# Kernel optimization log

Measured on AMD Instinct MI355X. Metric: run time of the kernel, lower is better.

The kernel has to match this reference:

```python
import jax, jax.numpy as jnp
import numpy as np
from jax import lax

B, L = 16384, 32
HID, CIN = 8, 2
N_SUB = 2            # RK4 substeps per spline interval (fixed-step stand-in for torchcde's adaptive solver)
T10_LO, T10_HI = 0.1, 7.0


def push_zeros(a):
    # torch: move nonzero entries of each row to the right end, zeros to the left.
    # stable ascending sort on validity key (0 for zeros, 1 for valid) reproduces this exactly
    # because the invalid entries are exactly 0.
    keys = (a != 0).astype(jnp.int32)
    order = jnp.argsort(keys, axis=1)  # jax sorts are stable
    return jnp.take_along_axis(a, order, axis=1)


def setup_inputs() -> dict:
    key = jax.random.key(0)
    ks = jax.random.split(key, 12)
    fa_len = jax.random.randint(ks[0], (B, 1), L // 2, L + 1)          # 16..32 valid points
    valid = jnp.arange(L)[None, :] < fa_len                             # (B, L)
    X_fa_in = jnp.where(valid, jax.random.uniform(ks[1], (B, L), minval=0.1, maxval=1.1), 0.0)
    fa_vals_in = jnp.where(valid, jax.random.uniform(ks[2], (B, L), minval=0.05, maxval=0.45), 0.0)
    TR_vals = jax.random.uniform(ks[3], (B, 1), minval=0.003, maxval=0.01)
    fa_mask = valid

    def lin(k, fout, fin):
        kw, kb = jax.random.split(k)
        s = 1.0 / np.sqrt(fin)
        return (jax.random.uniform(kw, (fout, fin), minval=-s, maxval=s),
                jax.random.uniform(kb, (fout,), minval=-s, maxval=s))

    W_init, b_init = lin(ks[4], HID, CIN)        # self.initial: Linear(2, 8)
    W1, b1 = lin(ks[5], 256, HID)                # CDE_Func.linear1
    W2, b2 = lin(ks[6], CIN * HID, 256)          # CDE_Func.linear2
    Wr1, br1 = lin(ks[7], 200, HID)              # reg_T10
    Wr2, br2 = lin(ks[8], 200, 200)
    Wr3, br3 = lin(ks[9], 1, 200)
    return dict(X_fa_in=X_fa_in, fa_vals_in=fa_vals_in, TR_vals=TR_vals,
                W_init=W_init, b_init=b_init, W1=W1, b1=b1, W2=W2, b2=b2,
                Wr1=Wr1, br1=br1, Wr2=Wr2, br2=br2, Wr3=Wr3, br3=br3,
                fa_mask=fa_mask, fa_len=fa_len)


def _forward(X_fa_in, fa_vals_in, TR_vals, W_init, b_init, W1, b1, W2, b2,
             Wr1, br1, Wr2, br2, Wr3, br3, fa_mask, fa_len):
    fl = fa_len[:, 0]                       # (B,) int
    fl_f = fl.astype(X_fa_in.dtype)
    mean = jnp.sum(X_fa_in, axis=1) / fl_f
    Xn = X_fa_in / mean[:, None]
    X_fa = push_zeros(Xn)
    fa_vals = push_zeros(fa_vals_in)
    bidx = jnp.arange(X_fa.shape[0])
    last_X = X_fa[bidx, fl - 1][:, None]            # pushed array indexed at fa_len-1 (as in torch)
    last_fa = fa_vals_in[bidx, fl - 1][:, None]     # original array indexed at fa_len-1
    X_fa = jnp.where(X_fa == 0.0, last_X, X_fa)
    fa_vals = jnp.where(fa_vals == 0.0, last_fa, fa_vals)
    x = jnp.stack([fa_vals, X_fa], axis=-1)         # (B, L, 2): channels (fa, X)

    # Hermite cubic with backward differences, unit knot spacing t_i = i
    diffs = x[:, 1:] - x[:, :-1]                    # (B, L-1, C)
    m = jnp.concatenate([diffs[:, :1], diffs], axis=1)  # m_0 = fwd diff, m_i = backward diff
    X0s, X1s = x[:, :-1], x[:, 1:]                  # per-interval knot values (B, L-1, C)
    M0s, M1s = m[:, :-1], m[:, 1:]

    z0 = x[:, 0] @ W_init.T + b_init                # X.evaluate(interval[0]) == first knot

    def f(z):  # CDE vector field: (B, HID) -> (B, HID, CIN)
        h = jax.nn.relu(z @ W1.T + b1)
        g = jnp.tanh(h @ W2.T + b2)
        return g.reshape(z.shape[0], HID, CIN)

    hstep = 1.0 / N_SUB
    nI = x.shape[1] - 1
    intervals = jnp.repeat(jnp.arange(nI), N_SUB)
    s0s = jnp.tile(jnp.arange(N_SUB) * hstep, nI).astype(x.dtype)

    def step(z, ts):
        i, s0 = ts
        x0, x1 = X0s[:, i], X1s[:, i]
        m0, m1 = M0s[:, i], M1s[:, i]

        def dX(s):  # spline derivative dX/dt at local coord s in [0,1]
            s2 = s * s
            return ((6 * s2 - 6 * s) * x0 + (3 * s2 - 4 * s + 1) * m0 +
                    (-6 * s2 + 6 * s) * x1 + (3 * s2 - 2 * s) * m1)

        def F(s, zz):
            return jnp.einsum('bhc,bc->bh', f(zz), dX(s))

        k1 = F(s0, z)
        k2 = F(s0 + hstep / 2, z + 0.5 * hstep * k1)
        k3 = F(s0 + hstep / 2, z + 0.5 * hstep * k2)
        k4 = F(s0 + hstep, z + hstep * k3)
        return z + (hstep / 6) * (k1 + 2 * k2 + 2 * k3 + k4), None

    z_T, _ = lax.scan(step, z0, (intervals, s0s))

    h1 = jax.nn.gelu(z_T @ Wr1.T + br1, approximate=False)
    h2 = jax.nn.gelu(h1 @ Wr2.T + br2, approximate=False)
    t = (h2 @ Wr3.T + br3)[:, 0]
    T10 = T10_LO + jax.nn.sigmoid(t)[:, None] * (T10_HI - T10_LO)   # (B, 1)
    R1 = 1.0 / T10
    E = jnp.exp(-TR_vals * R1)                                      # (B, 1)
    X_out = (1 - E) * jnp.sin(fa_vals_in) / (1 - jnp.cos(fa_vals_in) * E)
    mean2 = jnp.sum(X_out, axis=1) / fl_f
    X_out = X_out / mean2[:, None]
    M0 = jnp.ones_like(T10)
    return X_out, T10, M0


def reference(X_fa_in, fa_vals_in, TR_vals, W_init, b_init, W1, b1, W2, b2,
              Wr1, br1, Wr2, br2, Wr3, br3, fa_mask, fa_len):
    return _forward(X_fa_in, fa_vals_in, TR_vals, W_init, b_init, W1, b1, W2, b2,
                    Wr1, br1, Wr2, br2, Wr3, br3, fa_mask, fa_len)
```

## Files before the change

kernel.cpp:

```cpp
#include <hip/hip_runtime.h>
#include <hip/hip_bf16.h>

#define B_ROWS 16384
#define L_SEQ  32

typedef _Float16 f16;
typedef __attribute__((ext_vector_type(4))) _Float16 f16x4;
typedef __attribute__((ext_vector_type(8))) _Float16 f16x8;
typedef __attribute__((ext_vector_type(4))) float f32x4;
typedef __attribute__((ext_vector_type(4))) unsigned int u32x4;

__device__ __forceinline__ unsigned pkh(float a, float b) {
    return __builtin_bit_cast(unsigned, __builtin_amdgcn_cvt_pkrtz(a, b));
}
__device__ __forceinline__ float tanh_fast(float x) {
    float e = __expf(2.0f * x);
    float r = __builtin_amdgcn_rcpf(e + 1.0f);
    return fmaf(-2.0f, r, 1.0f);
}
__device__ __forceinline__ float gelu_exact(float x) {
    return 0.5f * x * (1.0f + erff(x * 0.70710678118654752440f));
}
__device__ __forceinline__ void pin2(uint2& v) {
    unsigned x0 = v.x, x1 = v.y;
    asm volatile("" : "+v"(x0), "+v"(x1));
    v = make_uint2(x0, x1);
}
__device__ __forceinline__ void pin4(u32x4& v) {
    unsigned x0 = v[0], x1 = v[1], x2 = v[2], x3 = v[3];
    asm volatile("" : "+v"(x0), "+v"(x1), "+v"(x2), "+v"(x3));
    v = (u32x4){x0, x1, x2, x3};
}

__global__ __launch_bounds__(256, 2) void fused_kernel(
    const float* __restrict__ Xin, const float* __restrict__ Fin,
    const float* __restrict__ TRv,
    const int*   __restrict__ fa_len,
    const float* __restrict__ Wi,  const float* __restrict__ bi,
    const float* __restrict__ W1g, const float* __restrict__ b1g,
    const float* __restrict__ W2g, const float* __restrict__ b2g,
    const float* __restrict__ Wr1, const float* __restrict__ br1,
    const float* __restrict__ Wr2, const float* __restrict__ br2,
    const float* __restrict__ Wr3, const float* __restrict__ br3,
    float* __restrict__ out)
{
    __shared__ __align__(16) float xm[32 * 132];
    __shared__ __align__(16) f32x4 exch[2][2][2][64];
    __shared__ float texch[2][2][16];
#define XM(r_, i_, c_) xm[(r_) * 132 + (i_) * 4 + (c_)]

    const int tid = threadIdx.x;
    const int g16 = tid >> 4, sub = tid & 15;

    float mean_r[2]; int fl_r[2];
#pragma unroll
    for (int r = 0; r < 2; ++r) {
        const int row_l = g16 * 2 + r;
        const int row   = blockIdx.x * 32 + row_l;
        const float* Xr = Xin + row * L_SEQ;
        const float* Fr = Fin + row * L_SEQ;
        float xr0 = Xr[sub], xr1 = Xr[sub + 16];
        float fr0 = Fr[sub], fr1 = Fr[sub + 16];
        fl_r[r] = fa_len[row];
        float s = xr0 + xr1;
        s += __shfl_xor(s, 1, 16);
        s += __shfl_xor(s, 2, 16);
        s += __shfl_xor(s, 4, 16);
        s += __shfl_xor(s, 8, 16);
        mean_r[r] = s / (float)fl_r[r];
        XM(row_l, sub, 0)      = fr0; XM(row_l, sub, 1)      = xr0;
        XM(row_l, sub + 16, 0) = fr1; XM(row_l, sub + 16, 1) = xr1;
    }
    __syncthreads();

    float ff[2][2], xf[2][2];
#pragma unroll
    for (int r = 0; r < 2; ++r) {
        const int row_l = g16 * 2 + r;
        const int fl = fl_r[r];
        const float mean = mean_r[r];
        const int shift = L_SEQ - fl;
        int lsrc  = fl - 1 - shift;
        int lsrcC = lsrc < 0 ? 0 : lsrc;
        float lastX = (lsrc >= 0) ? (XM(row_l, lsrcC, 1) / mean) : 0.0f;
        float lastF = XM(row_l, fl - 1, 0);
#pragma unroll
        for (int u = 0; u < 2; ++u) {
            int p = sub + u * 16;
            int src = p - shift;
            int sc  = src < 0 ? 0 : src;
            float fraw = XM(row_l, sc, 0);
            float xraw = XM(row_l, sc, 1);
            ff[r][u] = (src >= 0) ? fraw : lastF;
            xf[r][u] = (src >= 0) ? (xraw / mean) : lastX;
        }
    }
    __syncthreads();
#pragma unroll
    for (int r = 0; r < 2; ++r) {
        const int row_l = g16 * 2 + r;
#pragma unroll
        for (int u = 0; u < 2; ++u) {
            int p = sub + u * 16;
            XM(row_l, p, 0) = ff[r][u];
            XM(row_l, p, 1) = xf[r][u];
        }
    }
    __syncthreads();
#pragma unroll
    for (int r = 0; r < 2; ++r) {
        const int row_l = g16 * 2 + r;
#pragma unroll
        for (int u = 0; u < 2; ++u) {
            int p = sub + u * 16;
            int qd = (p == 0) ? 1 : p;
            XM(row_l, p, 2) = XM(row_l, qd, 0) - XM(row_l, qd - 1, 0);
            XM(row_l, p, 3) = XM(row_l, qd, 1) - XM(row_l, qd - 1, 1);
        }
    }
    __syncthreads();

    const int wv   = tid >> 6;
    const int lane = tid & 63;
    const int pairId = wv >> 1;
    const int half   = wv & 1;
    const int n    = lane & 15;
    const int q    = lane >> 4;
    const int rowl = pairId * 16 + n;
    const int rowg = blockIdx.x * 32 + rowl;

    uint2 a1[8];
#pragma unroll
    for (int tt = 0; tt < 8; ++tt) {
        const int t = 8 * half + tt;
        const float* wr = W1g + (t * 16 + n) * 8 + (q < 2 ? q * 4 : 0);
        float4 w4 = *(const float4*)wr;
        float b1v = b1g[t * 16 + n];
        unsigned d0 = (q < 2) ? pkh(w4.x, w4.y) : (q == 2 ? pkh(b1v, 0.0f) : 0u);
        unsigned d1 = (q < 2) ? pkh(w4.z, w4.w) : 0u;
        a1[tt] = make_uint2(d0, d1);
        pin2(a1[tt]);
    }
    u32x4 a2[4];
#pragma unroll
    for (int tt = 0; tt < 4; ++tt) {
        const int kk = 4 * half + tt;
        const float* w2r = W2g + n * 256 + kk * 32 + 4 * q;
        float4 p0 = *(const float4*)(w2r);
        float4 p1 = *(const float4*)(w2r + 16);
        a2[tt] = (u32x4){pkh(p0.x, p0.y), pkh(p0.z, p0.w), pkh(p1.x, p1.y), pkh(p1.z, p1.w)};
        pin4(a2[tt]);
    }
    f32x4 c2seed;
#pragma unroll
    for (int r = 0; r < 4; ++r) c2seed[r] = (half == 0) ? b2g[4 * q + r] : 0.0f;

    float f0 = XM(rowl, 0, 0), X0 = XM(rowl, 0, 1);
    float z0 = fmaf(Wi[(2 * q) * 2], f0, fmaf(Wi[(2 * q) * 2 + 1], X0, bi[2 * q]));
    float z1 = fmaf(Wi[(2 * q + 1) * 2], f0, fmaf(Wi[(2 * q + 1) * 2 + 1], X0, bi[2 * q + 1]));

    const int bpi = (((q & 1) << 5) + n) << 2;
    const f32x4 zero4 = {0.f, 0.f, 0.f, 0.f};
    const f16x8 zf16 = {0, 0, 0, 0, 0, 0, 0, 0};

    auto make_bz = [&](float zza, float zzb) -> uint2 {
        unsigned myz = pkh(zza, zzb);
        int b0 = __builtin_amdgcn_ds_bpermute(bpi, (int)myz);
        int b1 = __builtin_amdgcn_ds_bpermute(bpi + 64, (int)myz);
        unsigned bz0 = (q < 2) ? (unsigned)b0 : (q == 2 ? 0x3C00u : 0u);
        unsigned bz1 = (q < 2) ? (unsigned)b1 : 0u;
        return make_uint2(bz0, bz1);
    };

    auto FEVAL = [&](int ph, float zza, float zzb, float d0c, float d1c,
                     float& ko0, float& ko1) {
        uint2 bzp = make_bz(zza, zzb);
        f16x4 bz = __builtin_bit_cast(f16x4, bzp);

        f32x4 c1[8];
#pragma unroll
        for (int tt = 0; tt < 8; ++tt)
            c1[tt] = __builtin_amdgcn_mfma_f32_16x16x16f16(
                __builtin_bit_cast(f16x4, a1[tt]), bz, zero4, 0, 0, 0);

        f16x8 hf[4];
#pragma unroll
        for (int tt = 0; tt < 4; ++tt) {
            u32x4 w = (u32x4){pkh(c1[2 * tt][0],     c1[2 * tt][1]),
                              pkh(c1[2 * tt][2],     c1[2 * tt][3]),
                              pkh(c1[2 * tt + 1][0], c1[2 * tt + 1][1]),
                              pkh(c1[2 * tt + 1][2], c1[2 * tt + 1][3])};
            hf[tt] = __builtin_elementwise_max(__builtin_bit_cast(f16x8, w), zf16);
        }

        f32x4 c2a = c2seed, c2b = zero4;
        c2a = __builtin_amdgcn_mfma_f32_16x16x32_f16(
            __builtin_bit_cast(f16x8, a2[0]), hf[0], c2a, 0, 0, 0);
        c2b = __builtin_amdgcn_mfma_f32_16x16x32_f16(
            __builtin_bit_cast(f16x8, a2[2]), hf[2], c2b, 0, 0, 0);
        c2a = __builtin_amdgcn_mfma_f32_16x16x32_f16(
            __builtin_bit_cast(f16x8, a2[1]), hf[1], c2a, 0, 0, 0);
        c2b = __builtin_amdgcn_mfma_f32_16x16x32_f16(
            __builtin_bit_cast(f16x8, a2[3]), hf[3], c2b, 0, 0, 0);
        f32x4 Gp = c2a + c2b;

        exch[pairId][ph][half][lane] = Gp;
        __syncthreads();
        f32x4 G = Gp + exch[pairId][ph][half ^ 1][lane];

        float t0 = tanh_fast(G[0]), t1 = tanh_fast(G[1]);
        float t2 = tanh_fast(G[2]), t3 = tanh_fast(G[3]);
        ko0 = fmaf(t0, d0c, t1 * d1c);
        ko1 = fmaf(t2, d0c, t3 * d1c);
    };

    int ph = 0;
#pragma unroll 1
    for (int i = 0; i < 31; ++i) {
        float4 P0 = *(const float4*)&XM(rowl, i, 0);
        float4 P1 = *(const float4*)&XM(rowl, i + 1, 0);
        float m0f = P0.z, m0X = P0.w, m1f = P1.z, m1X = P1.w;
        float df  = P0.x - P1.x, dXx = P0.y - P1.y;

        float d25f = fmaf(-1.125f, df,  fmaf(0.1875f, m0f, -0.3125f * m1f));
        float d25X = fmaf(-1.125f, dXx, fmaf(0.1875f, m0X, -0.3125f * m1X));
        float d50f = fmaf(-1.5f,   df,  fmaf(-0.25f,  m0f, -0.25f   * m1f));
        float d50X = fmaf(-1.5f,   dXx, fmaf(-0.25f,  m0X, -0.25f   * m1X));
        float d75f = fmaf(-1.125f, df,  fmaf(-0.3125f, m0f, 0.1875f * m1f));
        float d75X = fmaf(-1.125f, dXx, fmaf(-0.3125f, m0X, 0.1875f * m1X));

#pragma unroll 1
        for (int ssi = 0; ssi < 2; ++ssi) {
            float daf = ssi ? d50f : m0f,  daX = ssi ? d50X : m0X;
            float dbf = ssi ? d75f : d25f, dbX = ssi ? d75X : d25X;
            float ddf = ssi ? m1f  : d50f, ddX = ssi ? m1X  : d50X;

            float k1a, k1b, k2a, k2b, k3a, k3b, k4a, k4b, zza, zzb;
            FEVAL(ph, z0, z1, daf, daX, k1a, k1b);       ph ^= 1;
            zza = fmaf(0.25f, k1a, z0); zzb = fmaf(0.25f, k1b, z1);
            FEVAL(ph, zza, zzb, dbf, dbX, k2a, k2b);     ph ^= 1;
            zza = fmaf(0.25f, k2a, z0); zzb = fmaf(0.25f, k2b, z1);
            FEVAL(ph, zza, zzb, dbf, dbX, k3a, k3b);     ph ^= 1;
            zza = fmaf(0.5f, k3a, z0);  zzb = fmaf(0.5f, k3b, z1);
            FEVAL(ph, zza, zzb, ddf, ddX, k4a, k4b);     ph ^= 1;

            float ka = fmaf(2.f, k2a, k1a); ka = fmaf(2.f, k3a, ka);
            float kb = fmaf(2.f, k2b, k1b); kb = fmaf(2.f, k3b, kb);
            z0 = fmaf(1.f / 12.f, ka + k4a, z0);
            z1 = fmaf(1.f / 12.f, kb + k4b, z1);
        }
    }

    uint2 bzp = make_bz(z0, z1);
    f16x4 bzr = __builtin_bit_cast(f16x4, bzp);
    f32x4 c1r[13];
#pragma unroll
    for (int t = 0; t < 13; ++t) {
        int m = 16 * t + n;
        uint2 afp = make_uint2(0u, 0u);
        if (q < 2) {
            if (m < 200) {
                float4 w4 = *(const float4*)(Wr1 + m * 8 + 4 * q);
                afp = make_uint2(pkh(w4.x, w4.y), pkh(w4.z, w4.w));
            }
        } else if (q == 2) {
            float b = (m < 200) ? br1[m] : 0.0f;
            afp.x = pkh(b, 0.0f);
        }
        c1r[t] = __builtin_amdgcn_mfma_f32_16x16x16f16(
            __builtin_bit_cast(f16x4, afp), bzr, zero4, 0, 0, 0);
    }

    f16x8 hf2[7];
#pragma unroll
    for (int kk = 0; kk < 7; ++kk) {
        float g0 = gelu_exact(c1r[2 * kk][0]), g1 = gelu_exact(c1r[2 * kk][1]);
        float g2 = gelu_exact(c1r[2 * kk][2]), g3 = gelu_exact(c1r[2 * kk][3]);
        float g4 = 0.f, g5 = 0.f, g6 = 0.f, g7 = 0.f;
        if (kk < 6) {
            g4 = gelu_exact(c1r[2 * kk + 1][0]); g5 = gelu_exact(c1r[2 * kk + 1][1]);
            g6 = gelu_exact(c1r[2 * kk + 1][2]); g7 = gelu_exact(c1r[2 * kk + 1][3]);
        }
        u32x4 w = (u32x4){pkh(g0, g1), pkh(g2, g3), pkh(g4, g5), pkh(g6, g7)};
        hf2[kk] = __builtin_bit_cast(f16x8, w);
    }

    float tpart = 0.0f;
    const int mt0 = half * 7, mt1 = half ? 13 : 7;
#pragma unroll 1
    for (int mt = mt0; mt < mt1; ++mt) {
        int mb = 16 * mt + 4 * q;
        f32x4 c2 = zero4;
        if (mb + 3 < 200) c2 = *(const f32x4*)(br2 + mb);
        int m2 = 16 * mt + n;
#pragma unroll
        for (int kk = 0; kk < 7; ++kk) {
            u32x4 af = {0u, 0u, 0u, 0u};
            if (m2 < 200) {
                int k0 = 32 * kk + 4 * q;
                const float* wr = Wr2 + m2 * 200 + k0;
                if (k0 + 3 < 200) {
                    float4 wa = *(const float4*)(wr);
                    af[0] = pkh(wa.x, wa.y); af[1] = pkh(wa.z, wa.w);
                }
                if (k0 + 19 < 200) {
                    float4 wb = *(const float4*)(wr + 16);
                    af[2] = pkh(wb.x, wb.y); af[3] = pkh(wb.z, wb.w);
                }
            }
            c2 = __builtin_amdgcn_mfma_f32_16x16x32_f16(
                __builtin_bit_cast(f16x8, af), hf2[kk], c2, 0, 0, 0);
        }
        float4 w3 = make_float4(0.f, 0.f, 0.f, 0.f);
        if (mb + 3 < 200) w3 = *(const float4*)(Wr3 + mb);
        tpart = fmaf(w3.x, gelu_exact(c2[0]), tpart);
        tpart = fmaf(w3.y, gelu_exact(c2[1]), tpart);
        tpart = fmaf(w3.z, gelu_exact(c2[2]), tpart);
        tpart = fmaf(w3.w, gelu_exact(c2[3]), tpart);
    }
    tpart += __shfl_xor(tpart, 16);
    tpart += __shfl_xor(tpart, 32);
    if (lane < 16) texch[pairId][half][n] = tpart;
    __syncthreads();
    float tval = texch[pairId][0][n] + texch[pairId][1][n] + br3[0];

    float sig  = __fdividef(1.0f, 1.0f + __expf(-tval));
    float T10  = 0.1f + 6.9f * sig;
    float E    = __expf(-TRv[rowg] * __builtin_amdgcn_rcpf(T10));

    const float* Fr = Fin + rowg * 32 + 8 * q;
    float xo[8]; float ssum = 0.0f;
#pragma unroll
    for (int j = 0; j < 8; ++j) {
        float fa = Fr[j];
        float sn = __sinf(fa), cs = __cosf(fa);
        float v = __fdividef((1.0f - E) * sn, 1.0f - cs * E);
        xo[j] = v; ssum += v;
    }
    ssum += __shfl_xor(ssum, 16);
    ssum += __shfl_xor(ssum, 32);
    float mean2 = ssum / (float)fa_len[rowg];
    float inv   = __fdividef(1.0f, mean2);

    if (half == 0) {
        float4* dst = (float4*)(out + rowg * 32 + 8 * q);
        dst[0] = make_float4(xo[0] * inv, xo[1] * inv, xo[2] * inv, xo[3] * inv);
        dst[1] = make_float4(xo[4] * inv, xo[5] * inv, xo[6] * inv, xo[7] * inv);
        if (q == 0) {
            out[B_ROWS * L_SEQ + rowg] = T10;
            out[B_ROWS * L_SEQ + B_ROWS + rowg] = 1.0f;
        }
    }
#undef XM
}

extern "C" void kernel_launch(void* const* d_in, const int* in_sizes, int n_in,
                              void* d_out, int out_size, void* d_ws, size_t ws_size,
                              hipStream_t stream) {
    const float* Xin  = (const float*)d_in[0];
    const float* Fin  = (const float*)d_in[1];
    const float* TRv  = (const float*)d_in[2];
    const float* Wi   = (const float*)d_in[3];
    const float* bi   = (const float*)d_in[4];
    const float* W1g  = (const float*)d_in[5];
    const float* b1g  = (const float*)d_in[6];
    const float* W2g  = (const float*)d_in[7];
    const float* b2g  = (const float*)d_in[8];
    const float* Wr1  = (const float*)d_in[9];
    const float* br1  = (const float*)d_in[10];
    const float* Wr2  = (const float*)d_in[11];
    const float* br2  = (const float*)d_in[12];
    const float* Wr3  = (const float*)d_in[13];
    const float* br3  = (const float*)d_in[14];
    const int*   flen = (const int*)d_in[16];

    float* outp = (float*)d_out;
    (void)d_ws; (void)ws_size;

    fused_kernel<<<dim3(B_ROWS / 32), dim3(256), 0, stream>>>(
        Xin, Fin, TRv, flen, Wi, bi, W1g, b1g, W2g, b2g,
        Wr1, br1, Wr2, br2, Wr3, br3, outp);
}
```

Before: 244.5 us.

## Split each 16-row group's hidden layer across four waves instead of two

Each block now handles 16 rows with four waves, and each wave owns a quarter of the 256-wide hidden layer instead of half. Partial outputs are summed through shared memory across the four waves, and the grid size doubles. Fewer MFMAs per wave and fewer held weight registers allow a higher launch-bounds occupancy target, shortening the serial RK4 critical path per row. In exchange, each function evaluation needs a four-way reduction and a block barrier, and the epilogue runs on only one wave.

```diff
diff --git a/kernel.cpp b/kernel.cpp
--- a/kernel.cpp
+++ b/kernel.cpp
@@ -32,7 +32,7 @@
     v = (u32x4){x0, x1, x2, x3};
 }
 
-__global__ __launch_bounds__(256, 2) void fused_kernel(
+__global__ __launch_bounds__(256, 4) void fused_kernel(
     const float* __restrict__ Xin, const float* __restrict__ Fin,
     const float* __restrict__ TRv,
     const int*   __restrict__ fa_len,
@@ -44,95 +44,75 @@
     const float* __restrict__ Wr3, const float* __restrict__ br3,
     float* __restrict__ out)
 {
-    __shared__ __align__(16) float xm[32 * 132];
-    __shared__ __align__(16) f32x4 exch[2][2][2][64];
-    __shared__ float texch[2][2][16];
+    __shared__ __align__(16) float xm[16 * 132];
+    __shared__ __align__(16) f32x4 exch[2][4][64];
+    __shared__ float texch[4][16];
 #define XM(r_, i_, c_) xm[(r_) * 132 + (i_) * 4 + (c_)]
 
     const int tid = threadIdx.x;
     const int g16 = tid >> 4, sub = tid & 15;
 
-    float mean_r[2]; int fl_r[2];
-#pragma unroll
-    for (int r = 0; r < 2; ++r) {
-        const int row_l = g16 * 2 + r;
-        const int row   = blockIdx.x * 32 + row_l;
-        const float* Xr = Xin + row * L_SEQ;
-        const float* Fr = Fin + row * L_SEQ;
+    {
+        const int prow = blockIdx.x * 16 + g16;
+        const float* Xr = Xin + prow * L_SEQ;
+        const float* Fr = Fin + prow * L_SEQ;
         float xr0 = Xr[sub], xr1 = Xr[sub + 16];
         float fr0 = Fr[sub], fr1 = Fr[sub + 16];
-        fl_r[r] = fa_len[row];
+        const int fl = fa_len[prow];
         float s = xr0 + xr1;
         s += __shfl_xor(s, 1, 16);
         s += __shfl_xor(s, 2, 16);
         s += __shfl_xor(s, 4, 16);
         s += __shfl_xor(s, 8, 16);
-        mean_r[r] = s / (float)fl_r[r];
-        XM(row_l, sub, 0)      = fr0; XM(row_l, sub, 1)      = xr0;
-        XM(row_l, sub + 16, 0) = fr1; XM(row_l, sub + 16, 1) = xr1;
-    }
-    __syncthreads();
-
-    float ff[2][2], xf[2][2];
-#pragma unroll
-    for (int r = 0; r < 2; ++r) {
-        const int row_l = g16 * 2 + r;
-        const int fl = fl_r[r];
-        const float mean = mean_r[r];
+        const float mean = s / (float)fl;
+        XM(g16, sub, 0)      = fr0; XM(g16, sub, 1)      = xr0;
+        XM(g16, sub + 16, 0) = fr1; XM(g16, sub + 16, 1) = xr1;
+        __syncthreads();
+
         const int shift = L_SEQ - fl;
         int lsrc  = fl - 1 - shift;
         int lsrcC = lsrc < 0 ? 0 : lsrc;
-        float lastX = (lsrc >= 0) ? (XM(row_l, lsrcC, 1) / mean) : 0.0f;
-        float lastF = XM(row_l, fl - 1, 0);
+        float lastX = (lsrc >= 0) ? (XM(g16, lsrcC, 1) / mean) : 0.0f;
+        float lastF = XM(g16, fl - 1, 0);
+        float ffv[2], xfv[2];
 #pragma unroll
         for (int u = 0; u < 2; ++u) {
             int p = sub + u * 16;
             int src = p - shift;
             int sc  = src < 0 ? 0 : src;
-            float fraw = XM(row_l, sc, 0);
-            float xraw = XM(row_l, sc, 1);
-            ff[r][u] = (src >= 0) ? fraw : lastF;
-            xf[r][u] = (src >= 0) ? (xraw / mean) : lastX;
-        }
-    }
-    __syncthreads();
-#pragma unroll
-    for (int r = 0; r < 2; ++r) {
-        const int row_l = g16 * 2 + r;
+            float fraw = XM(g16, sc, 0);
+            float xraw = XM(g16, sc, 1);
+            ffv[u] = (src >= 0) ? fraw : lastF;
+            xfv[u] = (src >= 0) ? (xraw / mean) : lastX;
+        }
+        __syncthreads();
 #pragma unroll
         for (int u = 0; u < 2; ++u) {
             int p = sub + u * 16;
-            XM(row_l, p, 0) = ff[r][u];
-            XM(row_l, p, 1) = xf[r][u];
-        }
-    }
-    __syncthreads();
-#pragma unroll
-    for (int r = 0; r < 2; ++r) {
-        const int row_l = g16 * 2 + r;
+            XM(g16, p, 0) = ffv[u];
+            XM(g16, p, 1) = xfv[u];
+        }
+        __syncthreads();
 #pragma unroll
         for (int u = 0; u < 2; ++u) {
             int p = sub + u * 16;
             int qd = (p == 0) ? 1 : p;
-            XM(row_l, p, 2) = XM(row_l, qd, 0) - XM(row_l, qd - 1, 0);
-            XM(row_l, p, 3) = XM(row_l, qd, 1) - XM(row_l, qd - 1, 1);
-        }
-    }
-    __syncthreads();
+            XM(g16, p, 2) = XM(g16, qd, 0) - XM(g16, qd - 1, 0);
+            XM(g16, p, 3) = XM(g16, qd, 1) - XM(g16, qd - 1, 1);
+        }
+        __syncthreads();
+    }
 
     const int wv   = tid >> 6;
     const int lane = tid & 63;
-    const int pairId = wv >> 1;
-    const int half   = wv & 1;
     const int n    = lane & 15;
     const int q    = lane >> 4;
-    const int rowl = pairId * 16 + n;
-    const int rowg = blockIdx.x * 32 + rowl;
-
-    uint2 a1[8];
-#pragma unroll
-    for (int tt = 0; tt < 8; ++tt) {
-        const int t = 8 * half + tt;
+    const int rowg = blockIdx.x * 16 + n;
+
+    uint2 a1[4];
+#pragma unroll
+    for (int tt = 0; tt < 4; ++tt) {
+        const int t = 4 * wv + tt;
         const float* wr = W1g + (t * 16 + n) * 8 + (q < 2 ? q * 4 : 0);
         float4 w4 = *(const float4*)wr;
         float b1v = b1g[t * 16 + n];
@@ -141,10 +121,10 @@
         a1[tt] = make_uint2(d0, d1);
         pin2(a1[tt]);
     }
-    u32x4 a2[4];
-#pragma unroll
-    for (int tt = 0; tt < 4; ++tt) {
-        const int kk = 4 * half + tt;
+    u32x4 a2[2];
+#pragma unroll
+    for (int tt = 0; tt < 2; ++tt) {
+        const int kk = 2 * wv + tt;
         const float* w2r = W2g + n * 256 + kk * 32 + 4 * q;
         float4 p0 = *(const float4*)(w2r);
         float4 p1 = *(const float4*)(w2r + 16);
@@ -153,9 +133,9 @@
     }
     f32x4 c2seed;
 #pragma unroll
-    for (int r = 0; r < 4; ++r) c2seed[r] = (half == 0) ? b2g[4 * q + r] : 0.0f;
-
-    float f0 = XM(rowl, 0, 0), X0 = XM(rowl, 0, 1);
+    for (int r = 0; r < 4; ++r) c2seed[r] = (wv == 0) ? b2g[4 * q + r] : 0.0f;
+
+    float f0 = XM(n, 0, 0), X0 = XM(n, 0, 1);
     float z0 = fmaf(Wi[(2 * q) * 2], f0, fmaf(Wi[(2 * q) * 2 + 1], X0, bi[2 * q]));
     float z1 = fmaf(Wi[(2 * q + 1) * 2], f0, fmaf(Wi[(2 * q + 1) * 2 + 1], X0, bi[2 * q + 1]));
 
@@ -177,15 +157,15 @@
         uint2 bzp = make_bz(zza, zzb);
         f16x4 bz = __builtin_bit_cast(f16x4, bzp);
 
-        f32x4 c1[8];
-#pragma unroll
-        for (int tt = 0; tt < 8; ++tt)
+        f32x4 c1[4];
+#pragma unroll
+        for (int tt = 0; tt < 4; ++tt)
             c1[tt] = __builtin_amdgcn_mfma_f32_16x16x16f16(
                 __builtin_bit_cast(f16x4, a1[tt]), bz, zero4, 0, 0, 0);
 
-        f16x8 hf[4];
-#pragma unroll
-        for (int tt = 0; tt < 4; ++tt) {
+        f16x8 hf[2];
+#pragma unroll
+        for (int tt = 0; tt < 2; ++tt) {
             u32x4 w = (u32x4){pkh(c1[2 * tt][0],     c1[2 * tt][1]),
                               pkh(c1[2 * tt][2],     c1[2 * tt][3]),
                               pkh(c1[2 * tt + 1][0], c1[2 * tt + 1][1]),
@@ -193,20 +173,16 @@
             hf[tt] = __builtin_elementwise_max(__builtin_bit_cast(f16x8, w), zf16);
         }
 
-        f32x4 c2a = c2seed, c2b = zero4;
-        c2a = __builtin_amdgcn_mfma_f32_16x16x32_f16(
-            __builtin_bit_cast(f16x8, a2[0]), hf[0], c2a, 0, 0, 0);
-        c2b = __builtin_amdgcn_mfma_f32_16x16x32_f16(
-            __builtin_bit_cast(f16x8, a2[2]), hf[2], c2b, 0, 0, 0);
-        c2a = __builtin_amdgcn_mfma_f32_16x16x32_f16(
-            __builtin_bit_cast(f16x8, a2[1]), hf[1], c2a, 0, 0, 0);
-        c2b = __builtin_amdgcn_mfma_f32_16x16x32_f16(
-            __builtin_bit_cast(f16x8, a2[3]), hf[3], c2b, 0, 0, 0);
-        f32x4 Gp = c2a + c2b;
-
-        exch[pairId][ph][half][lane] = Gp;
-        __syncthreads();
-        f32x4 G = Gp + exch[pairId][ph][half ^ 1][lane];
+        f32x4 c2 = c2seed;
+        c2 = __builtin_amdgcn_mfma_f32_16x16x32_f16(
+            __builtin_bit_cast(f16x8, a2[0]), hf[0], c2, 0, 0, 0);
+        c2 = __builtin_amdgcn_mfma_f32_16x16x32_f16(
+            __builtin_bit_cast(f16x8, a2[1]), hf[1], c2, 0, 0, 0);
+
+        exch[ph][wv][lane] = c2;
+        __syncthreads();
+        f32x4 G = ((exch[ph][0][lane] + exch[ph][1][lane])
+                 +  exch[ph][2][lane]) + exch[ph][3][lane];
 
         float t0 = tanh_fast(G[0]), t1 = tanh_fast(G[1]);
         float t2 = tanh_fast(G[2]), t3 = tanh_fast(G[3]);
@@ -217,8 +193,8 @@
     int ph = 0;
 #pragma unroll 1
     for (int i = 0; i < 31; ++i) {
-        float4 P0 = *(const float4*)&XM(rowl, i, 0);
-        float4 P1 = *(const float4*)&XM(rowl, i + 1, 0);
+        float4 P0 = *(const float4*)&XM(n, i, 0);
+        float4 P1 = *(const float4*)&XM(n, i + 1, 0);
         float m0f = P0.z, m0X = P0.w, m1f = P1.z, m1X = P1.w;
         float df  = P0.x - P1.x, dXx = P0.y - P1.y;
 
@@ -286,9 +262,8 @@
     }
 
     float tpart = 0.0f;
-    const int mt0 = half * 7, mt1 = half ? 13 : 7;
 #pragma unroll 1
-    for (int mt = mt0; mt < mt1; ++mt) {
+    for (int mt = wv; mt < 13; mt += 4) {
         int mb = 16 * mt + 4 * q;
         f32x4 c2 = zero4;
         if (mb + 3 < 200) c2 = *(const f32x4*)(br2 + mb);
@@ -320,29 +295,29 @@
     }
     tpart += __shfl_xor(tpart, 16);
     tpart += __shfl_xor(tpart, 32);
-    if (lane < 16) texch[pairId][half][n] = tpart;
+    if (lane < 16) texch[wv][n] = tpart;
     __syncthreads();
-    float tval = texch[pairId][0][n] + texch[pairId][1][n] + br3[0];
-
-    float sig  = __fdividef(1.0f, 1.0f + __expf(-tval));
-    float T10  = 0.1f + 6.9f * sig;
-    float E    = __expf(-TRv[rowg] * __builtin_amdgcn_rcpf(T10));
-
-    const float* Fr = Fin + rowg * 32 + 8 * q;
-    float xo[8]; float ssum = 0.0f;
-#pragma unroll
-    for (int j = 0; j < 8; ++j) {
-        float fa = Fr[j];
-        float sn = __sinf(fa), cs = __cosf(fa);
-        float v = __fdividef((1.0f - E) * sn, 1.0f - cs * E);
-        xo[j] = v; ssum += v;
-    }
-    ssum += __shfl_xor(ssum, 16);
-    ssum += __shfl_xor(ssum, 32);
-    float mean2 = ssum / (float)fa_len[rowg];
-    float inv   = __fdividef(1.0f, mean2);
-
-    if (half == 0) {
+
+    if (wv == 0) {
+        float tval = ((texch[0][n] + texch[1][n]) + texch[2][n]) + texch[3][n] + br3[0];
+        float sig  = __fdividef(1.0f, 1.0f + __expf(-tval));
+        float T10  = 0.1f + 6.9f * sig;
+        float E    = __expf(-TRv[rowg] * __builtin_amdgcn_rcpf(T10));
+
+        const float* Fr = Fin + rowg * 32 + 8 * q;
+        float xo[8]; float ssum = 0.0f;
+#pragma unroll
+        for (int j = 0; j < 8; ++j) {
+            float fa = Fr[j];
+            float sn = __sinf(fa), cs = __cosf(fa);
+            float v = __fdividef((1.0f - E) * sn, 1.0f - cs * E);
+            xo[j] = v; ssum += v;
+        }
+        ssum += __shfl_xor(ssum, 16);
+        ssum += __shfl_xor(ssum, 32);
+        float mean2 = ssum / (float)fa_len[rowg];
+        float inv   = __fdividef(1.0f, mean2);
+
         float4* dst = (float4*)(out + rowg * 32 + 8 * q);
         dst[0] = make_float4(xo[0] * inv, xo[1] * inv, xo[2] * inv, xo[3] * inv);
         dst[1] = make_float4(xo[4] * inv, xo[5] * inv, xo[6] * inv, xo[7] * inv);
@@ -377,7 +352,7 @@
     float* outp = (float*)d_out;
     (void)d_ws; (void)ws_size;
 
-    fused_kernel<<<dim3(B_ROWS / 32), dim3(256), 0, stream>>>(
+    fused_kernel<<<dim3(B_ROWS / 16), dim3(256), 0, stream>>>(
         Xin, Fin, TRv, flen, Wi, bi, W1g, b1g, W2g, b2g,
         Wr1, br1, Wr2, br2, Wr3, br3, outp);
 }
```

Result: slower. 286.8 us (+17.3%).
